# Kernel optimization log

Hardware: AMD Instinct MI355X
Metric: run time of the kernel (lower is better)

Reference implementation:

```python
import jax, jax.numpy as jnp
import numpy as np

N = 50000        # nodes
K = 16           # neighbors per node
F_IN = 140       # raw feature dim
H, D = 8, 16     # heads, head_dim -> hidden 128
L = 2            # GAT layers
HID = H * D
NEG_SLOPE = 0.2  # LeakyReLU slope in standard GAT


def setup_inputs() -> dict:
    key = jax.random.key(0)
    ks = jax.random.split(key, 8)
    feature = jax.random.normal(ks[0], (N, F_IN), dtype=jnp.float32)
    nb_id = jax.random.randint(ks[1], (N, K), 0, N)
    pca_w = jax.random.normal(ks[2], (F_IN, HID), dtype=jnp.float32) * (1.0 / np.sqrt(F_IN))
    pca_b = jax.random.normal(ks[3], (HID,), dtype=jnp.float32) * 0.01
    Ws = jax.random.normal(ks[4], (L, HID, HID), dtype=jnp.float32) * (1.0 / np.sqrt(HID))
    bs = jax.random.normal(ks[5], (L, HID), dtype=jnp.float32) * 0.01
    a_src = jax.random.normal(ks[6], (L, H, D), dtype=jnp.float32) * (1.0 / np.sqrt(D))
    a_dst = jax.random.normal(ks[7], (L, H, D), dtype=jnp.float32) * (1.0 / np.sqrt(D))
    return {"feature": feature, "nb_id": nb_id, "pca_w": pca_w, "pca_b": pca_b,
            "Ws": Ws, "bs": bs, "a_src": a_src, "a_dst": a_dst}


def _gat_layer(x, nb_id, W, b, asrc, adst):
    # x: [N, HID] -> per-head features h: [N, H, D]
    h = (x @ W + b).reshape(-1, H, D)
    s_src = jnp.einsum('nhd,hd->nh', h, asrc)          # [N, H]
    s_dst = jnp.einsum('nhd,hd->nh', h, adst)          # [N, H]
    # attention logits over K neighbors: [N, K, H]
    e = jax.nn.leaky_relu(s_src[:, None, :] + s_dst[nb_id], NEG_SLOPE)
    alpha = jax.nn.softmax(e, axis=1)                  # softmax over neighbors
    # gather neighbor features [N, K, H, D] and aggregate
    out = jnp.einsum('nkh,nkhd->nhd', alpha, h[nb_id])
    return jax.nn.elu(out.reshape(-1, HID))


def reference(feature, nb_id, pca_w, pca_b, Ws, bs, a_src, a_dst):
    # SparseInput: dropout is identity in eval mode
    x = jax.nn.relu(feature @ pca_w + pca_b)           # [N, HID]
    for l in range(L):
        x = _gat_layer(x, nb_id, Ws[l], bs[l], a_src[l], a_dst[l])
    return x
```

## Files before the change

kernel.cpp:

```cpp
#include <hip/hip_runtime.h>
#include <math.h>

#define NN 50000
#define KK 16
#define FIN 140
#define HH 8
#define HID 128

typedef __attribute__((ext_vector_type(8))) short short8;
typedef __attribute__((ext_vector_type(4))) float f32x4;

__device__ inline unsigned short f2bf(float f) {
  unsigned int u = __float_as_uint(f);
  return (unsigned short)((u + 0x7fffu + ((u >> 16) & 1u)) >> 16);
}
__device__ inline float bf2f(unsigned short h) {
  return __uint_as_float(((unsigned int)h) << 16);
}

__global__ __launch_bounds__(256) void prep_kernel(
    const float* __restrict__ pca_w, const float* __restrict__ Ws,
    unsigned short* __restrict__ frags) {
  const int gid = blockIdx.x * 256 + threadIdx.x;
  const float* W; int K; unsigned short *dh, *dl; int tid;
  if (gid < 20480)      { W = pca_w;          K = FIN; dh = frags;                 dl = dh + 20480; tid = gid; }
  else if (gid < 36864) { W = Ws;             K = HID; dh = frags + 40960;         dl = dh + 16384; tid = gid - 20480; }
  else                  { W = Ws + HID * HID; K = HID; dh = frags + 40960 + 32768; dl = dh + 16384; tid = gid - 36864; }
  const int j = tid & 7, L = (tid >> 3) & 63, ct = tid >> 9, t = ct & 7, c = ct >> 3;
  const int k = c * 32 + (L >> 4) * 8 + j;
  const int col = t * 16 + (L & 15);
  const float v = (k < K) ? W[(size_t)k * HID + col] : 0.f;
  const unsigned short h = f2bf(v);
  dh[tid] = h;
  dl[tid] = f2bf(v - bf2f(h));
}

__global__ __launch_bounds__(64) void pca_mfma(
    const float* __restrict__ feat, const unsigned short* __restrict__ wfh,
    const unsigned short* __restrict__ wfl, const float* __restrict__ b,
    unsigned short* __restrict__ xbf) {
  const int lane = threadIdx.x;
  const int col = lane & 15, quad = lane >> 4;
  const int tile0 = blockIdx.x * 2;
  const int tile1 = tile0 + 1;
  const bool has1 = (tile1 < NN / 16);
  const int n0 = tile0 * 16, n1 = tile1 * 16;
  f32x4 acc0[8], acc1[8];
#pragma unroll
  for (int t = 0; t < 8; ++t) {
    acc0[t] = (f32x4){0.f, 0.f, 0.f, 0.f};
    acc1[t] = (f32x4){0.f, 0.f, 0.f, 0.f};
  }
  const float* brow0 = feat + (size_t)(n0 + col) * FIN + quad * 8;
  const float* brow1 = feat + (size_t)((has1 ? n1 : n0) + col) * FIN + quad * 8;
#pragma unroll
  for (int c = 0; c < 5; ++c) {
    float4 a0, a1, c0, c1;
    if (c < 4) {
      a0 = *(const float4*)(brow0 + c * 32);
      a1 = *(const float4*)(brow0 + c * 32 + 4);
      c0 = *(const float4*)(brow1 + c * 32);
      c1 = *(const float4*)(brow1 + c * 32 + 4);
    } else {
      a0 = make_float4(0.f, 0.f, 0.f, 0.f); a1 = a0; c0 = a0; c1 = a0;
      if (quad == 0) {
        a0 = *(const float4*)(brow0 + 128); a1 = *(const float4*)(brow0 + 132);
        c0 = *(const float4*)(brow1 + 128); c1 = *(const float4*)(brow1 + 132);
      } else if (quad == 1) {
        a0 = *(const float4*)(brow0 + 128);
        c0 = *(const float4*)(brow1 + 128);
      }
    }
    short8 B0, B1;
    B0[0] = (short)f2bf(a0.x); B0[1] = (short)f2bf(a0.y);
    B0[2] = (short)f2bf(a0.z); B0[3] = (short)f2bf(a0.w);
    B0[4] = (short)f2bf(a1.x); B0[5] = (short)f2bf(a1.y);
    B0[6] = (short)f2bf(a1.z); B0[7] = (short)f2bf(a1.w);
    B1[0] = (short)f2bf(c0.x); B1[1] = (short)f2bf(c0.y);
    B1[2] = (short)f2bf(c0.z); B1[3] = (short)f2bf(c0.w);
    B1[4] = (short)f2bf(c1.x); B1[5] = (short)f2bf(c1.y);
    B1[6] = (short)f2bf(c1.z); B1[7] = (short)f2bf(c1.w);
#pragma unroll
    for (int t = 0; t < 8; ++t) {
      const short8 Ah = *(const short8*)(wfh + ((size_t)(c * 8 + t) * 64 + lane) * 8);
      const short8 Al = *(const short8*)(wfl + ((size_t)(c * 8 + t) * 64 + lane) * 8);
      acc0[t] = __builtin_amdgcn_mfma_f32_16x16x32_bf16(Al, B0, acc0[t], 0, 0, 0);
      acc0[t] = __builtin_amdgcn_mfma_f32_16x16x32_bf16(Ah, B0, acc0[t], 0, 0, 0);
      acc1[t] = __builtin_amdgcn_mfma_f32_16x16x32_bf16(Al, B1, acc1[t], 0, 0, 0);
      acc1[t] = __builtin_amdgcn_mfma_f32_16x16x32_bf16(Ah, B1, acc1[t], 0, 0, 0);
    }
  }
#pragma unroll
  for (int t = 0; t < 8; ++t) {
    const float4 bv = *(const float4*)(b + t * 16 + quad * 4);
    {
      const float v0 = fmaxf(acc0[t][0] + bv.x, 0.f);
      const float v1 = fmaxf(acc0[t][1] + bv.y, 0.f);
      const float v2 = fmaxf(acc0[t][2] + bv.z, 0.f);
      const float v3 = fmaxf(acc0[t][3] + bv.w, 0.f);
      uint2 pk;
      pk.x = (unsigned)f2bf(v0) | ((unsigned)f2bf(v1) << 16);
      pk.y = (unsigned)f2bf(v2) | ((unsigned)f2bf(v3) << 16);
      *(uint2*)&xbf[(size_t)(n0 + col) * HID + t * 16 + quad * 4] = pk;
    }
    if (has1) {
      const float v0 = fmaxf(acc1[t][0] + bv.x, 0.f);
      const float v1 = fmaxf(acc1[t][1] + bv.y, 0.f);
      const float v2 = fmaxf(acc1[t][2] + bv.z, 0.f);
      const float v3 = fmaxf(acc1[t][3] + bv.w, 0.f);
      uint2 pk;
      pk.x = (unsigned)f2bf(v0) | ((unsigned)f2bf(v1) << 16);
      pk.y = (unsigned)f2bf(v2) | ((unsigned)f2bf(v3) << 16);
      *(uint2*)&xbf[(size_t)(n1 + col) * HID + t * 16 + quad * 4] = pk;
    }
  }
}

__global__ __launch_bounds__(64) void proj_mfma(
    const unsigned short* __restrict__ xbf, const unsigned short* __restrict__ wfh,
    const unsigned short* __restrict__ wfl, const float* __restrict__ b,
    const float* __restrict__ asrc, const float* __restrict__ adst,
    unsigned short* __restrict__ hbf, float* __restrict__ ssrc,
    float* __restrict__ sdst) {
  const int lane = threadIdx.x;
  const int col = lane & 15, quad = lane >> 4;
  const int tile0 = blockIdx.x * 2;
  const int tile1 = tile0 + 1;
  const bool has1 = (tile1 < NN / 16);
  const int n0 = tile0 * 16, n1 = tile1 * 16;
  f32x4 acc0[8], acc1[8];
#pragma unroll
  for (int t = 0; t < 8; ++t) {
    acc0[t] = (f32x4){0.f, 0.f, 0.f, 0.f};
    acc1[t] = (f32x4){0.f, 0.f, 0.f, 0.f};
  }
  const unsigned short* brow0 = xbf + (size_t)(n0 + col) * HID + quad * 8;
  const unsigned short* brow1 = xbf + (size_t)((has1 ? n1 : n0) + col) * HID + quad * 8;
  short8 B0[4], B1[4];
#pragma unroll
  for (int c = 0; c < 4; ++c) {
    B0[c] = *(const short8*)(brow0 + c * 32);
    B1[c] = *(const short8*)(brow1 + c * 32);
  }
#pragma unroll
  for (int c = 0; c < 4; ++c) {
#pragma unroll
    for (int t = 0; t < 8; ++t) {
      const short8 Ah = *(const short8*)(wfh + ((size_t)(c * 8 + t) * 64 + lane) * 8);
      const short8 Al = *(const short8*)(wfl + ((size_t)(c * 8 + t) * 64 + lane) * 8);
      acc0[t] = __builtin_amdgcn_mfma_f32_16x16x32_bf16(Al, B0[c], acc0[t], 0, 0, 0);
      acc0[t] = __builtin_amdgcn_mfma_f32_16x16x32_bf16(Ah, B0[c], acc0[t], 0, 0, 0);
      acc1[t] = __builtin_amdgcn_mfma_f32_16x16x32_bf16(Al, B1[c], acc1[t], 0, 0, 0);
      acc1[t] = __builtin_amdgcn_mfma_f32_16x16x32_bf16(Ah, B1[c], acc1[t], 0, 0, 0);
    }
  }
#pragma unroll
  for (int t = 0; t < 8; ++t) {
    const float4 bv = *(const float4*)(b + t * 16 + quad * 4);
    const float4 av = *(const float4*)(asrc + t * 16 + quad * 4);
    const float4 dv = *(const float4*)(adst + t * 16 + quad * 4);
#pragma unroll
    for (int p = 0; p < 2; ++p) {
      if (p == 1 && !has1) break;
      const f32x4& a = p ? acc1[t] : acc0[t];
      const int nb_ = p ? n1 : n0;
      const float v0 = a[0] + bv.x;
      const float v1 = a[1] + bv.y;
      const float v2 = a[2] + bv.z;
      const float v3 = a[3] + bv.w;
      uint2 pk;
      pk.x = (unsigned)f2bf(v0) | ((unsigned)f2bf(v1) << 16);
      pk.y = (unsigned)f2bf(v2) | ((unsigned)f2bf(v3) << 16);
      *(uint2*)&hbf[(size_t)(nb_ + col) * HID + t * 16 + quad * 4] = pk;
      float ps = v0 * av.x + v1 * av.y + v2 * av.z + v3 * av.w;
      float pd = v0 * dv.x + v1 * dv.y + v2 * dv.z + v3 * dv.w;
      ps += __shfl_xor(ps, 16); ps += __shfl_xor(ps, 32);
      pd += __shfl_xor(pd, 16); pd += __shfl_xor(pd, 32);
      if (quad == 0) ssrc[(size_t)(nb_ + col) * HH + t] = ps;
      if (quad == 1) sdst[(size_t)(nb_ + col) * HH + t] = pd;
    }
  }
}

template <bool LAST>
__device__ inline void attn_body(
    const int* __restrict__ nb, const unsigned int* __restrict__ hbf,
    const float* __restrict__ ssrc, const float* __restrict__ sdst,
    void* __restrict__ xout, int lane, int wid, int nwaves) {
  for (int base = wid * 2; base < NN; base += nwaves * 2) {
    const int nA = base, nB = base + 1;
    int nbv = 0;
    if (lane < KK) nbv = nb[(size_t)nA * KK + lane];
    else if (lane < 2 * KK) nbv = nb[(size_t)nB * KK + (lane - KK)];
    unsigned int uA[KK], uB[KK];
#pragma unroll
    for (int k = 0; k < KK; ++k) {
      const int rA = __shfl(nbv, k);
      uA[k] = hbf[(size_t)rA * (HID / 2) + lane];
    }
#pragma unroll
    for (int k = 0; k < KK; ++k) {
      const int rB = __shfl(nbv, KK + k);
      uB[k] = hbf[(size_t)rB * (HID / 2) + lane];
    }
    const int h = lane & 7, k0 = lane >> 3;
    const int rA0 = __shfl(nbv, k0), rA1 = __shfl(nbv, k0 + 8);
    const int rB0 = __shfl(nbv, KK + k0), rB1 = __shfl(nbv, KK + k0 + 8);
    const float ssA = ssrc[(size_t)nA * HH + h];
    const float ssB = ssrc[(size_t)nB * HH + h];
    float eA0 = ssA + sdst[(size_t)rA0 * HH + h];
    float eA1 = ssA + sdst[(size_t)rA1 * HH + h];
    float eB0 = ssB + sdst[(size_t)rB0 * HH + h];
    float eB1 = ssB + sdst[(size_t)rB1 * HH + h];
    eA0 = eA0 > 0.f ? eA0 : 0.2f * eA0;
    eA1 = eA1 > 0.f ? eA1 : 0.2f * eA1;
    eB0 = eB0 > 0.f ? eB0 : 0.2f * eB0;
    eB1 = eB1 > 0.f ? eB1 : 0.2f * eB1;
    float mA = fmaxf(eA0, eA1), mB = fmaxf(eB0, eB1);
    mA = fmaxf(mA, __shfl_xor(mA, 8));  mB = fmaxf(mB, __shfl_xor(mB, 8));
    mA = fmaxf(mA, __shfl_xor(mA, 16)); mB = fmaxf(mB, __shfl_xor(mB, 16));
    mA = fmaxf(mA, __shfl_xor(mA, 32)); mB = fmaxf(mB, __shfl_xor(mB, 32));
    float pA0 = __expf(eA0 - mA), pA1 = __expf(eA1 - mA);
    float pB0 = __expf(eB0 - mB), pB1 = __expf(eB1 - mB);
    float sA = pA0 + pA1, sB = pB0 + pB1;
    sA += __shfl_xor(sA, 8);  sB += __shfl_xor(sB, 8);
    sA += __shfl_xor(sA, 16); sB += __shfl_xor(sB, 16);
    sA += __shfl_xor(sA, 32); sB += __shfl_xor(sB, 32);
    const float invA = 1.f / sA, invB = 1.f / sB;
    pA0 *= invA; pA1 *= invA; pB0 *= invB; pB1 *= invB;
    const int head = lane >> 3;
    float aA0 = 0.f, aA1 = 0.f, aB0 = 0.f, aB1 = 0.f;
#pragma unroll
    for (int k = 0; k < KK; ++k) {
      const float selA = (k < 8) ? pA0 : pA1;
      const float selB = (k < 8) ? pB0 : pB1;
      const float wA = __shfl(selA, ((k & 7) << 3) + head);
      const float wB = __shfl(selB, ((k & 7) << 3) + head);
      aA0 = fmaf(wA, __uint_as_float(uA[k] << 16), aA0);
      aA1 = fmaf(wA, __uint_as_float(uA[k] & 0xffff0000u), aA1);
      aB0 = fmaf(wB, __uint_as_float(uB[k] << 16), aB0);
      aB1 = fmaf(wB, __uint_as_float(uB[k] & 0xffff0000u), aB1);
    }
    const float oA0 = aA0 > 0.f ? aA0 : __expf(aA0) - 1.f;
    const float oA1 = aA1 > 0.f ? aA1 : __expf(aA1) - 1.f;
    const float oB0 = aB0 > 0.f ? aB0 : __expf(aB0) - 1.f;
    const float oB1 = aB1 > 0.f ? aB1 : __expf(aB1) - 1.f;
    if (LAST) {
      *(float2*)((float*)xout + (size_t)nA * HID + 2 * lane) = make_float2(oA0, oA1);
      *(float2*)((float*)xout + (size_t)nB * HID + 2 * lane) = make_float2(oB0, oB1);
    } else {
      ((unsigned int*)xout)[(size_t)nA * (HID / 2) + lane] =
          (unsigned)f2bf(oA0) | ((unsigned)f2bf(oA1) << 16);
      ((unsigned int*)xout)[(size_t)nB * (HID / 2) + lane] =
          (unsigned)f2bf(oB0) | ((unsigned)f2bf(oB1) << 16);
    }
  }
}

__global__ __launch_bounds__(256) void attn0_kernel(
    const int* __restrict__ nb, const unsigned int* __restrict__ hbf,
    const float* __restrict__ ssrc, const float* __restrict__ sdst,
    unsigned short* __restrict__ xbf) {
  const int lane = threadIdx.x & 63;
  const int wid = (blockIdx.x << 2) + (threadIdx.x >> 6);
  attn_body<false>(nb, hbf, ssrc, sdst, (void*)xbf, lane, wid, gridDim.x << 2);
}

__global__ __launch_bounds__(256) void attn1_kernel(
    const int* __restrict__ nb, const unsigned int* __restrict__ hbf,
    const float* __restrict__ ssrc, const float* __restrict__ sdst,
    float* __restrict__ out) {
  const int lane = threadIdx.x & 63;
  const int wid = (blockIdx.x << 2) + (threadIdx.x >> 6);
  attn_body<true>(nb, hbf, ssrc, sdst, (void*)out, lane, wid, gridDim.x << 2);
}

extern "C" void kernel_launch(void* const* d_in, const int* in_sizes, int n_in,
                              void* d_out, int out_size, void* d_ws, size_t ws_size,
                              hipStream_t stream) {
  const float* feature = (const float*)d_in[0];
  const int*   nb      = (const int*)d_in[1];
  const float* pca_w   = (const float*)d_in[2];
  const float* pca_b   = (const float*)d_in[3];
  const float* Ws      = (const float*)d_in[4];
  const float* bs      = (const float*)d_in[5];
  const float* a_src   = (const float*)d_in[6];
  const float* a_dst   = (const float*)d_in[7];
  float* out = (float*)d_out;

  unsigned short* xbf = (unsigned short*)d_ws;
  unsigned short* hbf = xbf + (size_t)NN * HID;
  float* ssrc = (float*)(hbf + (size_t)NN * HID);
  float* sdst = ssrc + (size_t)NN * HH;
  unsigned short* frags = (unsigned short*)(sdst + (size_t)NN * HH);

  const int ntile2 = (NN / 16 + 1) / 2;
  prep_kernel<<<208, 256, 0, stream>>>(pca_w, Ws, frags);
  pca_mfma<<<ntile2, 64, 0, stream>>>(feature, frags, frags + 20480, pca_b, xbf);
  for (int l = 0; l < 2; ++l) {
    const unsigned short* wh = frags + 40960 + (size_t)l * 32768;
    proj_mfma<<<ntile2, 64, 0, stream>>>(
        xbf, wh, wh + 16384, bs + (size_t)l * HID,
        a_src + (size_t)l * HID, a_dst + (size_t)l * HID, hbf, ssrc, sdst);
    if (l == 1)
      attn1_kernel<<<2048, 256, 0, stream>>>(nb, (const unsigned int*)hbf,
                                             ssrc, sdst, out);
    else
      attn0_kernel<<<2048, 256, 0, stream>>>(nb, (const unsigned int*)hbf,
                                             ssrc, sdst, xbf);
  }
}
```

Measured before the change: 206.2 us.

## Store projected features head-major and split attention across heads per block

The projection kernel now writes h, s_src and s_dst in a head-major layout ([H][N][16] and [H][N]). The attention kernel is restructured so each block handles one head, and each wave processes 8 nodes with 8 lanes per node. Each lane gathers a 32-byte head slice of each neighbor. The aim is locality: neighbor gathers for one head stay within a smaller per-head array (about 1.6 MB), which should improve cache hit rates. In exchange, each 256-byte neighbor row is split into eight separate 32-byte gathers, and neighbor indices are re-read once per head.

```diff
diff --git a/kernel.cpp b/kernel.cpp
--- a/kernel.cpp
+++ b/kernel.cpp
@@ -120,8 +120,8 @@
     const unsigned short* __restrict__ xbf, const unsigned short* __restrict__ wfh,
     const unsigned short* __restrict__ wfl, const float* __restrict__ b,
     const float* __restrict__ asrc, const float* __restrict__ adst,
-    unsigned short* __restrict__ hbf, float* __restrict__ ssrc,
-    float* __restrict__ sdst) {
+    unsigned short* __restrict__ hm, float* __restrict__ sm,
+    float* __restrict__ dm) {
   const int lane = threadIdx.x;
   const int col = lane & 15, quad = lane >> 4;
   const int tile0 = blockIdx.x * 2;
@@ -171,108 +171,88 @@
       uint2 pk;
       pk.x = (unsigned)f2bf(v0) | ((unsigned)f2bf(v1) << 16);
       pk.y = (unsigned)f2bf(v2) | ((unsigned)f2bf(v3) << 16);
-      *(uint2*)&hbf[(size_t)(nb_ + col) * HID + t * 16 + quad * 4] = pk;
+      *(uint2*)&hm[((size_t)t * NN + nb_ + col) * 16 + quad * 4] = pk;
       float ps = v0 * av.x + v1 * av.y + v2 * av.z + v3 * av.w;
       float pd = v0 * dv.x + v1 * dv.y + v2 * dv.z + v3 * dv.w;
       ps += __shfl_xor(ps, 16); ps += __shfl_xor(ps, 32);
       pd += __shfl_xor(pd, 16); pd += __shfl_xor(pd, 32);
-      if (quad == 0) ssrc[(size_t)(nb_ + col) * HH + t] = ps;
-      if (quad == 1) sdst[(size_t)(nb_ + col) * HH + t] = pd;
+      if (quad == 0) sm[(size_t)t * NN + nb_ + col] = ps;
+      if (quad == 1) dm[(size_t)t * NN + nb_ + col] = pd;
     }
   }
 }
 
 template <bool LAST>
 __device__ inline void attn_body(
-    const int* __restrict__ nb, const unsigned int* __restrict__ hbf,
-    const float* __restrict__ ssrc, const float* __restrict__ sdst,
-    void* __restrict__ xout, int lane, int wid, int nwaves) {
-  for (int base = wid * 2; base < NN; base += nwaves * 2) {
-    const int nA = base, nB = base + 1;
-    int nbv = 0;
-    if (lane < KK) nbv = nb[(size_t)nA * KK + lane];
-    else if (lane < 2 * KK) nbv = nb[(size_t)nB * KK + (lane - KK)];
-    unsigned int uA[KK], uB[KK];
-#pragma unroll
-    for (int k = 0; k < KK; ++k) {
-      const int rA = __shfl(nbv, k);
-      uA[k] = hbf[(size_t)rA * (HID / 2) + lane];
-    }
-#pragma unroll
-    for (int k = 0; k < KK; ++k) {
-      const int rB = __shfl(nbv, KK + k);
-      uB[k] = hbf[(size_t)rB * (HID / 2) + lane];
-    }
-    const int h = lane & 7, k0 = lane >> 3;
-    const int rA0 = __shfl(nbv, k0), rA1 = __shfl(nbv, k0 + 8);
-    const int rB0 = __shfl(nbv, KK + k0), rB1 = __shfl(nbv, KK + k0 + 8);
-    const float ssA = ssrc[(size_t)nA * HH + h];
-    const float ssB = ssrc[(size_t)nB * HH + h];
-    float eA0 = ssA + sdst[(size_t)rA0 * HH + h];
-    float eA1 = ssA + sdst[(size_t)rA1 * HH + h];
-    float eB0 = ssB + sdst[(size_t)rB0 * HH + h];
-    float eB1 = ssB + sdst[(size_t)rB1 * HH + h];
-    eA0 = eA0 > 0.f ? eA0 : 0.2f * eA0;
-    eA1 = eA1 > 0.f ? eA1 : 0.2f * eA1;
-    eB0 = eB0 > 0.f ? eB0 : 0.2f * eB0;
-    eB1 = eB1 > 0.f ? eB1 : 0.2f * eB1;
-    float mA = fmaxf(eA0, eA1), mB = fmaxf(eB0, eB1);
-    mA = fmaxf(mA, __shfl_xor(mA, 8));  mB = fmaxf(mB, __shfl_xor(mB, 8));
-    mA = fmaxf(mA, __shfl_xor(mA, 16)); mB = fmaxf(mB, __shfl_xor(mB, 16));
-    mA = fmaxf(mA, __shfl_xor(mA, 32)); mB = fmaxf(mB, __shfl_xor(mB, 32));
-    float pA0 = __expf(eA0 - mA), pA1 = __expf(eA1 - mA);
-    float pB0 = __expf(eB0 - mB), pB1 = __expf(eB1 - mB);
-    float sA = pA0 + pA1, sB = pB0 + pB1;
-    sA += __shfl_xor(sA, 8);  sB += __shfl_xor(sB, 8);
-    sA += __shfl_xor(sA, 16); sB += __shfl_xor(sB, 16);
-    sA += __shfl_xor(sA, 32); sB += __shfl_xor(sB, 32);
-    const float invA = 1.f / sA, invB = 1.f / sB;
-    pA0 *= invA; pA1 *= invA; pB0 *= invB; pB1 *= invB;
-    const int head = lane >> 3;
-    float aA0 = 0.f, aA1 = 0.f, aB0 = 0.f, aB1 = 0.f;
-#pragma unroll
-    for (int k = 0; k < KK; ++k) {
-      const float selA = (k < 8) ? pA0 : pA1;
-      const float selB = (k < 8) ? pB0 : pB1;
-      const float wA = __shfl(selA, ((k & 7) << 3) + head);
-      const float wB = __shfl(selB, ((k & 7) << 3) + head);
-      aA0 = fmaf(wA, __uint_as_float(uA[k] << 16), aA0);
-      aA1 = fmaf(wA, __uint_as_float(uA[k] & 0xffff0000u), aA1);
-      aB0 = fmaf(wB, __uint_as_float(uB[k] << 16), aB0);
-      aB1 = fmaf(wB, __uint_as_float(uB[k] & 0xffff0000u), aB1);
-    }
-    const float oA0 = aA0 > 0.f ? aA0 : __expf(aA0) - 1.f;
-    const float oA1 = aA1 > 0.f ? aA1 : __expf(aA1) - 1.f;
-    const float oB0 = aB0 > 0.f ? aB0 : __expf(aB0) - 1.f;
-    const float oB1 = aB1 > 0.f ? aB1 : __expf(aB1) - 1.f;
+    const int* __restrict__ nb, const unsigned int* __restrict__ hm,
+    const float* __restrict__ sm, const float* __restrict__ dm,
+    void* __restrict__ xout) {
+  const int lane = threadIdx.x & 63;
+  const int h = blockIdx.x & 7;
+  const int grp = (blockIdx.x >> 3) * 4 + (threadIdx.x >> 6);
+  const int n0 = grp * 8;
+  const int n8 = lane >> 3;
+  const int k8 = lane & 7;
+  const int nme = n0 + n8;
+  const int nc = nme < NN ? nme : NN - 1;
+  const int nbA = nb[(size_t)nc * KK + k8];
+  const int nbB = nb[(size_t)nc * KK + 8 + k8];
+  const unsigned int* hs = hm + (size_t)h * NN * 8;
+  unsigned int ug[16];
+#pragma unroll
+  for (int g = 0; g < 16; ++g) {
+    const int src = (lane & 0x38) + (g & 7);
+    const int r = __shfl((g < 8) ? nbA : nbB, src);
+    ug[g] = hs[(size_t)r * 8 + (lane & 7)];
+  }
+  const float ss = sm[(size_t)h * NN + nc];
+  float e0 = ss + dm[(size_t)h * NN + nbA];
+  float e1 = ss + dm[(size_t)h * NN + nbB];
+  e0 = e0 > 0.f ? e0 : 0.2f * e0;
+  e1 = e1 > 0.f ? e1 : 0.2f * e1;
+  float m = fmaxf(e0, e1);
+  m = fmaxf(m, __shfl_xor(m, 1));
+  m = fmaxf(m, __shfl_xor(m, 2));
+  m = fmaxf(m, __shfl_xor(m, 4));
+  float p0 = __expf(e0 - m), p1 = __expf(e1 - m);
+  float s = p0 + p1;
+  s += __shfl_xor(s, 1); s += __shfl_xor(s, 2); s += __shfl_xor(s, 4);
+  const float inv = 1.f / s;
+  p0 *= inv; p1 *= inv;
+  float a0 = 0.f, a1 = 0.f;
+#pragma unroll
+  for (int g = 0; g < 16; ++g) {
+    const int src = (lane & 0x38) + (g & 7);
+    const float w = __shfl((g < 8) ? p0 : p1, src);
+    a0 = fmaf(w, __uint_as_float(ug[g] << 16), a0);
+    a1 = fmaf(w, __uint_as_float(ug[g] & 0xffff0000u), a1);
+  }
+  const float o0 = a0 > 0.f ? a0 : __expf(a0) - 1.f;
+  const float o1 = a1 > 0.f ? a1 : __expf(a1) - 1.f;
+  if (nme < NN) {
+    const int u = lane & 7;
     if (LAST) {
-      *(float2*)((float*)xout + (size_t)nA * HID + 2 * lane) = make_float2(oA0, oA1);
-      *(float2*)((float*)xout + (size_t)nB * HID + 2 * lane) = make_float2(oB0, oB1);
+      *(float2*)((float*)xout + (size_t)nme * HID + h * 16 + 2 * u) =
+          make_float2(o0, o1);
     } else {
-      ((unsigned int*)xout)[(size_t)nA * (HID / 2) + lane] =
-          (unsigned)f2bf(oA0) | ((unsigned)f2bf(oA1) << 16);
-      ((unsigned int*)xout)[(size_t)nB * (HID / 2) + lane] =
-          (unsigned)f2bf(oB0) | ((unsigned)f2bf(oB1) << 16);
+      ((unsigned int*)xout)[(size_t)nme * (HID / 2) + h * 8 + u] =
+          (unsigned)f2bf(o0) | ((unsigned)f2bf(o1) << 16);
     }
   }
 }
 
 __global__ __launch_bounds__(256) void attn0_kernel(
-    const int* __restrict__ nb, const unsigned int* __restrict__ hbf,
-    const float* __restrict__ ssrc, const float* __restrict__ sdst,
+    const int* __restrict__ nb, const unsigned int* __restrict__ hm,
+    const float* __restrict__ sm, const float* __restrict__ dm,
     unsigned short* __restrict__ xbf) {
-  const int lane = threadIdx.x & 63;
-  const int wid = (blockIdx.x << 2) + (threadIdx.x >> 6);
-  attn_body<false>(nb, hbf, ssrc, sdst, (void*)xbf, lane, wid, gridDim.x << 2);
+  attn_body<false>(nb, hm, sm, dm, (void*)xbf);
 }
 
 __global__ __launch_bounds__(256) void attn1_kernel(
-    const int* __restrict__ nb, const unsigned int* __restrict__ hbf,
-    const float* __restrict__ ssrc, const float* __restrict__ sdst,
+    const int* __restrict__ nb, const unsigned int* __restrict__ hm,
+    const float* __restrict__ sm, const float* __restrict__ dm,
     float* __restrict__ out) {
-  const int lane = threadIdx.x & 63;
-  const int wid = (blockIdx.x << 2) + (threadIdx.x >> 6);
-  attn_body<true>(nb, hbf, ssrc, sdst, (void*)out, lane, wid, gridDim.x << 2);
+  attn_body<true>(nb, hm, sm, dm, (void*)out);
 }
 
 extern "C" void kernel_launch(void* const* d_in, const int* in_sizes, int n_in,
@@ -289,24 +269,25 @@
   float* out = (float*)d_out;
 
   unsigned short* xbf = (unsigned short*)d_ws;
-  unsigned short* hbf = xbf + (size_t)NN * HID;
-  float* ssrc = (float*)(hbf + (size_t)NN * HID);
-  float* sdst = ssrc + (size_t)NN * HH;
-  unsigned short* frags = (unsigned short*)(sdst + (size_t)NN * HH);
+  unsigned short* hm  = xbf + (size_t)NN * HID;
+  float* sm = (float*)(hm + (size_t)HH * NN * 16);
+  float* dm = sm + (size_t)HH * NN;
+  unsigned short* frags = (unsigned short*)(dm + (size_t)HH * NN);
 
   const int ntile2 = (NN / 16 + 1) / 2;
+  const int nattn = ((NN + 31) / 32) * 8;
   prep_kernel<<<208, 256, 0, stream>>>(pca_w, Ws, frags);
   pca_mfma<<<ntile2, 64, 0, stream>>>(feature, frags, frags + 20480, pca_b, xbf);
   for (int l = 0; l < 2; ++l) {
     const unsigned short* wh = frags + 40960 + (size_t)l * 32768;
     proj_mfma<<<ntile2, 64, 0, stream>>>(
         xbf, wh, wh + 16384, bs + (size_t)l * HID,
-        a_src + (size_t)l * HID, a_dst + (size_t)l * HID, hbf, ssrc, sdst);
+        a_src + (size_t)l * HID, a_dst + (size_t)l * HID, hm, sm, dm);
     if (l == 1)
-      attn1_kernel<<<2048, 256, 0, stream>>>(nb, (const unsigned int*)hbf,
-                                             ssrc, sdst, out);
+      attn1_kernel<<<nattn, 256, 0, stream>>>(nb, (const unsigned int*)hm,
+                                              sm, dm, out);
     else
-      attn0_kernel<<<2048, 256, 0, stream>>>(nb, (const unsigned int*)hbf,
-                                             ssrc, sdst, xbf);
-  }
-}
+      attn0_kernel<<<nattn, 256, 0, stream>>>(nb, (const unsigned int*)hm,
+                                              sm, dm, xbf);
+  }
+}
```

Result: slower. 240.0 us (+16.4%).
